# Performance work log

Measured on AMD Instinct MI355X. Metric: run time of the kernel, lower is better.

## Reference

```python
import jax, jax.numpy as jnp
import numpy as np

NUM_PARTS = 16
NUM_K = 256          # num_k_per_part; table rows per part = NUM_K + 1
VAE_DIMS = 768
OUT_DIMS = 1024
B = 4096


def setup_inputs() -> dict:
    key = jax.random.key(0)
    k0, k1, k2, k3, k4 = jax.random.split(key, 5)
    hashes = jax.random.randint(k0, (B, NUM_PARTS), 0, NUM_K + 1)  # values 0..256
    # nn.init.normal_(embedding.weight, 0.0, 0.01)
    emb = jax.random.normal(k1, ((NUM_K + 1) * NUM_PARTS, VAE_DIMS), dtype=jnp.float32) * 0.01
    # projection: Linear(768 -> 1024), ReLU, Linear(1024 -> 1024)
    W1 = jax.random.normal(k2, (VAE_DIMS, OUT_DIMS), dtype=jnp.float32) * (1.0 / np.sqrt(VAE_DIMS))
    b1 = jnp.zeros((OUT_DIMS,), dtype=jnp.float32)
    W2 = jax.random.normal(k3, (OUT_DIMS, OUT_DIMS), dtype=jnp.float32) * (1.0 / np.sqrt(OUT_DIMS))
    b2 = jnp.zeros((OUT_DIMS,), dtype=jnp.float32)
    # pe = randn(num_parts, out_dims) * 1.0
    pe = jax.random.normal(k4, (NUM_PARTS, OUT_DIMS), dtype=jnp.float32)
    return {"hashes": hashes, "emb": emb, "W1": W1, "b1": b1, "W2": W2, "b2": b2, "pe": pe}


def reference(hashes, emb, W1, b1, W2, b2, pe):
    # forward(hashes, index=None, get_mu=False, input_is_mu=False)
    offset = jnp.arange(NUM_PARTS, dtype=hashes.dtype) * (NUM_K + 1)  # [P]
    idx = hashes + offset[None, :]                                    # [B, P]
    mu = emb[idx]                                                     # [B, P, VAE]
    h = jax.nn.relu(jnp.einsum('bpv,vh->bph', mu, W1) + b1)           # [B, P, OUT]
    projected = jnp.einsum('bph,ho->bpo', h, W2) + b2                 # [B, P, OUT]
    return projected + pe[None, :, :]                                 # pe broadcast over batch
```

## Files before the change

kernel.cpp:

```cpp
#include <hip/hip_runtime.h>
#include <stdint.h>

#define NPARTS 16
#define NK1    257
#define ROWS   4112
#define MPAD   4224
#define VAE    768
#define ODIM   1024
#define BROWS  65536

typedef __attribute__((ext_vector_type(4))) float f32x4;
typedef __attribute__((ext_vector_type(8))) short s16x8;

static __device__ __forceinline__ unsigned short f2bf(float f) {
  union { float f; unsigned u; } v; v.f = f;
  unsigned x = v.u;
  unsigned r = x + 0x7FFFu + ((x >> 16) & 1u);
  return (unsigned short)(r >> 16);
}

static __device__ __forceinline__ void gload_lds16(const void* g, void* l) {
  __builtin_amdgcn_global_load_lds(
      (const __attribute__((address_space(1))) unsigned int*)g,
      (__attribute__((address_space(3))) unsigned int*)l, 16, 0, 0);
}

#define EMB_BLOCKS 1024
__global__ __launch_bounds__(256) void prep_kernel(
    const float* __restrict__ emb, const float* __restrict__ W1,
    unsigned short* __restrict__ embB, unsigned short* __restrict__ w1t) {
  __shared__ unsigned short tile[32][33];
  const int tid = threadIdx.x;
  const int bid = blockIdx.x;
  if (bid < EMB_BLOCKS) {
    const int NQ = MPAD * VAE / 4;
    for (int g = bid * 256 + tid; g < NQ; g += EMB_BLOCKS * 256) {
      const int i4 = g * 4;
      ushort4 o;
      if (i4 < ROWS * VAE) {
        const float4 v = *(const float4*)(emb + i4);
        o.x = f2bf(v.x); o.y = f2bf(v.y); o.z = f2bf(v.z); o.w = f2bf(v.w);
      } else {
        o.x = 0; o.y = 0; o.z = 0; o.w = 0;
      }
      *(ushort4*)(embB + i4) = o;
    }
  } else {
    const int tb = bid - EMB_BLOCKS;
    const int nkt = VAE / 32;
    const int tk = (tb % nkt) * 32;
    const int tn = (tb / nkt) * 32;
    const int r  = tid >> 3;
    const int c4 = (tid & 7) * 4;
    const float4 v = *(const float4*)(W1 + (size_t)(tk + r) * ODIM + tn + c4);
    tile[r][c4 + 0] = f2bf(v.x);
    tile[r][c4 + 1] = f2bf(v.y);
    tile[r][c4 + 2] = f2bf(v.z);
    tile[r][c4 + 3] = f2bf(v.w);
    __syncthreads();
    ushort4 o;
    o.x = tile[c4 + 0][r];
    o.y = tile[c4 + 1][r];
    o.z = tile[c4 + 2][r];
    o.w = tile[c4 + 3][r];
    *(ushort4*)(w1t + (size_t)(tn + r) * VAE + tk + c4) = o;
  }
}

template <int K, int MODE, bool DO_W2T>
__global__ __launch_bounds__(256) void gemm_kernel(
    const unsigned short* __restrict__ A, const unsigned short* __restrict__ BT,
    const float* __restrict__ bias, const float* __restrict__ pe,
    unsigned short* __restrict__ outB, float* __restrict__ outF,
    const float* __restrict__ W2src, unsigned short* __restrict__ w2dst) {
  __shared__ __align__(16) unsigned short smem[3 * 12288];
  const int tid = threadIdx.x;

  if (DO_W2T && blockIdx.z == 1) {
    if (blockIdx.y >= 32) return;
    unsigned short (*ttile)[132] = (unsigned short (*)[132])smem;
    const int tk = blockIdx.y * 32, tn = blockIdx.x * 128;
#pragma unroll
    for (int q = 0; q < 4; ++q) {
      const int row = (tid >> 5) + q * 8, c4 = (tid & 31) * 4;
      const float4 v = *(const float4*)(W2src + (size_t)(tk + row) * ODIM + tn + c4);
      ttile[row][c4 + 0] = f2bf(v.x); ttile[row][c4 + 1] = f2bf(v.y);
      ttile[row][c4 + 2] = f2bf(v.z); ttile[row][c4 + 3] = f2bf(v.w);
    }
    __syncthreads();
#pragma unroll
    for (int q = 0; q < 4; ++q) {
      const int n = (tid >> 3) + q * 32, k4 = (tid & 7) * 4;
      ushort4 o;
      o.x = ttile[k4 + 0][n]; o.y = ttile[k4 + 1][n];
      o.z = ttile[k4 + 2][n]; o.w = ttile[k4 + 3][n];
      *(ushort4*)(w2dst + (size_t)(tn + n) * ODIM + tk + k4) = o;
    }
    return;
  }

  const int lane = tid & 63;
  const int wave = tid >> 6;
  const int wc   = wave * 32;
  const int brow = blockIdx.y * 64;
  const int bcol = blockIdx.x * 128;
  const int la   = lane & 15;
  const int hi   = lane >> 4;

  f32x4 acc[4][2];
#pragma unroll
  for (int m = 0; m < 4; ++m)
#pragma unroll
    for (int n = 0; n < 2; ++n)
#pragma unroll
      for (int r = 0; r < 4; ++r) acc[m][n][r] = 0.f;

  const int srow = tid >> 3;
  const int skb  = (tid & 7) ^ (srow & 7);
  const unsigned short* gA = A + (size_t)(brow + srow) * K + skb * 8;
  const unsigned short* gB = BT + (size_t)(bcol + srow) * K + skb * 8;

#define STAGE(b, kt)                                              \
  {                                                               \
    unsigned short* la_ = smem + (b) * 12288 + tid * 8;           \
    unsigned short* lb_ = la_ + 4096;                             \
    gload_lds16(gA + (kt), la_);                                  \
    gload_lds16(gA + (kt) + 32 * K, la_ + 2048);                  \
    gload_lds16(gB + (kt), lb_);                                  \
    gload_lds16(gB + (kt) + 32 * K, lb_ + 2048);                  \
    gload_lds16(gB + (kt) + 64 * K, lb_ + 4096);                  \
    gload_lds16(gB + (kt) + 96 * K, lb_ + 6144);                  \
  }

  const int NT = K / 64;
  STAGE(0, 0);
  STAGE(1, 64);

#pragma unroll
  for (int t = 0; t < NT; ++t) {
    if (t < NT - 1) asm volatile("s_waitcnt vmcnt(6)" ::: "memory");
    else            asm volatile("s_waitcnt vmcnt(0)" ::: "memory");
    __builtin_amdgcn_sched_barrier(0);
    __builtin_amdgcn_s_barrier();
    if (t + 2 < NT) STAGE((t + 2) % 3, (t + 2) * 64);

    const unsigned short* As = smem + (t % 3) * 12288;
    const unsigned short* Bs = As + 4096;
    s16x8 af[4][2], bf[2][2];
#pragma unroll
    for (int m = 0; m < 4; ++m)
#pragma unroll
      for (int ks = 0; ks < 2; ++ks)
        af[m][ks] = *(const s16x8*)(As + (m * 16 + la) * 64 +
                                    (((ks * 4 + hi) ^ (la & 7)) * 8));
#pragma unroll
    for (int n = 0; n < 2; ++n)
#pragma unroll
      for (int ks = 0; ks < 2; ++ks)
        bf[n][ks] = *(const s16x8*)(Bs + (wc + n * 16 + la) * 64 +
                                    (((ks * 4 + hi) ^ (la & 7)) * 8));
    asm volatile("s_waitcnt lgkmcnt(0)" ::: "memory");
    __builtin_amdgcn_sched_barrier(0);

    __builtin_amdgcn_s_setprio(1);
#pragma unroll
    for (int m = 0; m < 4; ++m)
#pragma unroll
      for (int n = 0; n < 2; ++n)
#pragma unroll
        for (int ks = 0; ks < 2; ++ks)
          acc[m][n] = __builtin_amdgcn_mfma_f32_16x16x32_bf16(af[m][ks], bf[n][ks],
                                                              acc[m][n], 0, 0, 0);
    __builtin_amdgcn_s_setprio(0);
  }
#undef STAGE

#pragma unroll
  for (int m = 0; m < 4; ++m) {
    const int row0 = brow + m * 16 + hi * 4;
#pragma unroll
    for (int n = 0; n < 2; ++n) {
      const int col = bcol + wc + n * 16 + la;
      const float bv = bias[col];
      if (MODE == 0) {
#pragma unroll
        for (int r = 0; r < 4; ++r) {
          float v = acc[m][n][r] + bv;
          v = v > 0.f ? v : 0.f;
          outB[(size_t)(row0 + r) * ODIM + col] = f2bf(v);
        }
      } else {
#pragma unroll
        for (int r = 0; r < 4; ++r) {
          const int row = row0 + r;
          int p = row / NK1;
          if (p > NPARTS - 1) p = NPARTS - 1;
          outF[(size_t)row * ODIM + col] = acc[m][n][r] + bv + pe[(size_t)p * ODIM + col];
        }
      }
    }
  }
}

__global__ __launch_bounds__(256) void gather_kernel(const int* __restrict__ hashes,
                                                     const float* __restrict__ T,
                                                     float* __restrict__ out) {
  const int wid  = (blockIdx.x * blockDim.x + threadIdx.x) >> 6;
  const int lane = threadIdx.x & 63;
  const int nw   = (gridDim.x * blockDim.x) >> 6;
  for (int row = wid; row < BROWS; row += nw) {
    const int h = __builtin_amdgcn_readfirstlane(hashes[row]);
    const int p = row & (NPARTS - 1);
    const f32x4* __restrict__ src = (const f32x4*)(T + (size_t)(h + p * NK1) * ODIM);
    f32x4* __restrict__ dst = (f32x4*)(out + (size_t)row * ODIM);
#pragma unroll
    for (int j = 0; j < 4; ++j) {
      f32x4 v = src[lane + j * 64];
      __builtin_nontemporal_store(v, dst + lane + j * 64);
    }
  }
}

extern "C" void kernel_launch(void* const* d_in, const int* in_sizes, int n_in,
                              void* d_out, int out_size, void* d_ws, size_t ws_size,
                              hipStream_t stream) {
  const int*   hashes = (const int*)d_in[0];
  const float* emb    = (const float*)d_in[1];
  const float* W1     = (const float*)d_in[2];
  const float* b1     = (const float*)d_in[3];
  const float* W2     = (const float*)d_in[4];
  const float* b2     = (const float*)d_in[5];
  const float* pe     = (const float*)d_in[6];
  float* out = (float*)d_out;

  char* ws = (char*)d_ws;
  unsigned short* embB = (unsigned short*)(ws);
  unsigned short* w1t  = (unsigned short*)(ws + 6488064);
  unsigned short* w2t  = (unsigned short*)(ws + 8060928);
  unsigned short* H    = (unsigned short*)(ws + 10158080);
  float*          T    = (float*)(ws + 18808832);

  prep_kernel<<<EMB_BLOCKS + 768, 256, 0, stream>>>(emb, W1, embB, w1t);

  gemm_kernel<VAE, 0, true><<<dim3(8, 66, 2), 256, 0, stream>>>(
      embB, w1t, b1, nullptr, H, nullptr, W2, w2t);

  gemm_kernel<ODIM, 2, false><<<dim3(8, 66, 1), 256, 0, stream>>>(
      H, w2t, b2, pe, nullptr, T, nullptr, nullptr);

  gather_kernel<<<2048, 256, 0, stream>>>(hashes, T, out);
}
```

Before: 95.36 us.

## Fuse emb bf16 conversion into GEMM1, simplify pipelines, XCD-localize gather

The separate conversion of the embedding table to bf16 is removed; GEMM1 now reads fp32 emb rows directly, converts them in registers and writes swizzled bf16 into LDS, which saves one full read/write pass over the table. Both GEMMs go from a 3-stage global_load_lds pipeline with explicit waitcnt, setprio and sched_barrier to a simpler 2-stage double buffer using __syncthreads. The gather kernel is remapped so each group of blocks (blockIdx & 7, likely targeting one XCD) handles two parts, improving L2 locality on the T table. The cost is that the A operand now goes through register loads and conversion in the hot loop, and the pipeline is shallower.

```diff
diff --git a/kernel.cpp b/kernel.cpp
--- a/kernel.cpp
+++ b/kernel.cpp
@@ -25,58 +25,38 @@
       (__attribute__((address_space(3))) unsigned int*)l, 16, 0, 0);
 }
 
-#define EMB_BLOCKS 1024
 __global__ __launch_bounds__(256) void prep_kernel(
-    const float* __restrict__ emb, const float* __restrict__ W1,
-    unsigned short* __restrict__ embB, unsigned short* __restrict__ w1t) {
+    const float* __restrict__ W1, unsigned short* __restrict__ w1t) {
   __shared__ unsigned short tile[32][33];
   const int tid = threadIdx.x;
-  const int bid = blockIdx.x;
-  if (bid < EMB_BLOCKS) {
-    const int NQ = MPAD * VAE / 4;
-    for (int g = bid * 256 + tid; g < NQ; g += EMB_BLOCKS * 256) {
-      const int i4 = g * 4;
-      ushort4 o;
-      if (i4 < ROWS * VAE) {
-        const float4 v = *(const float4*)(emb + i4);
-        o.x = f2bf(v.x); o.y = f2bf(v.y); o.z = f2bf(v.z); o.w = f2bf(v.w);
-      } else {
-        o.x = 0; o.y = 0; o.z = 0; o.w = 0;
-      }
-      *(ushort4*)(embB + i4) = o;
-    }
-  } else {
-    const int tb = bid - EMB_BLOCKS;
-    const int nkt = VAE / 32;
-    const int tk = (tb % nkt) * 32;
-    const int tn = (tb / nkt) * 32;
-    const int r  = tid >> 3;
-    const int c4 = (tid & 7) * 4;
-    const float4 v = *(const float4*)(W1 + (size_t)(tk + r) * ODIM + tn + c4);
-    tile[r][c4 + 0] = f2bf(v.x);
-    tile[r][c4 + 1] = f2bf(v.y);
-    tile[r][c4 + 2] = f2bf(v.z);
-    tile[r][c4 + 3] = f2bf(v.w);
-    __syncthreads();
-    ushort4 o;
-    o.x = tile[c4 + 0][r];
-    o.y = tile[c4 + 1][r];
-    o.z = tile[c4 + 2][r];
-    o.w = tile[c4 + 3][r];
-    *(ushort4*)(w1t + (size_t)(tn + r) * VAE + tk + c4) = o;
-  }
-}
-
-template <int K, int MODE, bool DO_W2T>
-__global__ __launch_bounds__(256) void gemm_kernel(
-    const unsigned short* __restrict__ A, const unsigned short* __restrict__ BT,
-    const float* __restrict__ bias, const float* __restrict__ pe,
-    unsigned short* __restrict__ outB, float* __restrict__ outF,
+  const int tb  = blockIdx.x;
+  const int nkt = VAE / 32;
+  const int tk = (tb % nkt) * 32;
+  const int tn = (tb / nkt) * 32;
+  const int r  = tid >> 3;
+  const int c4 = (tid & 7) * 4;
+  const float4 v = *(const float4*)(W1 + (size_t)(tk + r) * ODIM + tn + c4);
+  tile[r][c4 + 0] = f2bf(v.x);
+  tile[r][c4 + 1] = f2bf(v.y);
+  tile[r][c4 + 2] = f2bf(v.z);
+  tile[r][c4 + 3] = f2bf(v.w);
+  __syncthreads();
+  ushort4 o;
+  o.x = tile[c4 + 0][r];
+  o.y = tile[c4 + 1][r];
+  o.z = tile[c4 + 2][r];
+  o.w = tile[c4 + 3][r];
+  *(ushort4*)(w1t + (size_t)(tn + r) * VAE + tk + c4) = o;
+}
+
+__global__ __launch_bounds__(256) void gemm1_kernel(
+    const float* __restrict__ emb, const unsigned short* __restrict__ BT,
+    const float* __restrict__ bias, unsigned short* __restrict__ outB,
     const float* __restrict__ W2src, unsigned short* __restrict__ w2dst) {
-  __shared__ __align__(16) unsigned short smem[3 * 12288];
+  __shared__ __align__(16) unsigned short smem[2 * 12288];
   const int tid = threadIdx.x;
 
-  if (DO_W2T && blockIdx.z == 1) {
+  if (blockIdx.z == 1) {
     if (blockIdx.y >= 32) return;
     unsigned short (*ttile)[132] = (unsigned short (*)[132])smem;
     const int tk = blockIdx.y * 32, tn = blockIdx.x * 128;
@@ -106,6 +86,115 @@
   const int bcol = blockIdx.x * 128;
   const int la   = lane & 15;
   const int hi   = lane >> 4;
+
+  f32x4 acc[4][2];
+#pragma unroll
+  for (int m = 0; m < 4; ++m)
+#pragma unroll
+    for (int n = 0; n < 2; ++n)
+#pragma unroll
+      for (int r = 0; r < 4; ++r) acc[m][n][r] = 0.f;
+
+  const int srow = tid >> 3;
+  const int skb  = (tid & 7) ^ (srow & 7);
+  const unsigned short* gB = BT + (size_t)(bcol + srow) * VAE + skb * 8;
+  const int arow = tid >> 2;
+  const int ak   = (tid & 3) * 16;
+  const int kb0  = ((tid & 3) * 2) ^ (arow & 7);
+  const int kb1  = ((tid & 3) * 2 + 1) ^ (arow & 7);
+  const bool aok = (brow + arow) < ROWS;
+  const float* gA = emb + (size_t)(brow + arow) * VAE + ak;
+
+  auto stage = [&](int b, int kt) {
+    unsigned short* lb_ = smem + b * 12288 + 4096 + tid * 8;
+    gload_lds16(gB + kt, lb_);
+    gload_lds16(gB + kt + 32 * VAE, lb_ + 2048);
+    gload_lds16(gB + kt + 64 * VAE, lb_ + 4096);
+    gload_lds16(gB + kt + 96 * VAE, lb_ + 6144);
+    float4 f0, f1, f2, f3;
+    if (aok) {
+      f0 = *(const float4*)(gA + kt);
+      f1 = *(const float4*)(gA + kt + 4);
+      f2 = *(const float4*)(gA + kt + 8);
+      f3 = *(const float4*)(gA + kt + 12);
+    } else {
+      f0 = f1 = f2 = f3 = float4{0.f, 0.f, 0.f, 0.f};
+    }
+    s16x8 p0, p1;
+    p0[0] = f2bf(f0.x); p0[1] = f2bf(f0.y); p0[2] = f2bf(f0.z); p0[3] = f2bf(f0.w);
+    p0[4] = f2bf(f1.x); p0[5] = f2bf(f1.y); p0[6] = f2bf(f1.z); p0[7] = f2bf(f1.w);
+    p1[0] = f2bf(f2.x); p1[1] = f2bf(f2.y); p1[2] = f2bf(f2.z); p1[3] = f2bf(f2.w);
+    p1[4] = f2bf(f3.x); p1[5] = f2bf(f3.y); p1[6] = f2bf(f3.z); p1[7] = f2bf(f3.w);
+    unsigned short* la_ = smem + b * 12288 + arow * 64;
+    *(s16x8*)(la_ + kb0 * 8) = p0;
+    *(s16x8*)(la_ + kb1 * 8) = p1;
+  };
+
+  stage(0, 0);
+  __syncthreads();
+
+  const int NT = VAE / 64;
+  for (int t = 0; t < NT; ++t) {
+    const int cur = t & 1;
+    if (t + 1 < NT) stage(cur ^ 1, (t + 1) * 64);
+
+    const unsigned short* As = smem + cur * 12288;
+    const unsigned short* Bs = As + 4096;
+    s16x8 af[4][2], bf[2][2];
+#pragma unroll
+    for (int m = 0; m < 4; ++m)
+#pragma unroll
+      for (int ks = 0; ks < 2; ++ks)
+        af[m][ks] = *(const s16x8*)(As + (m * 16 + la) * 64 +
+                                    (((ks * 4 + hi) ^ (la & 7)) * 8));
+#pragma unroll
+    for (int n = 0; n < 2; ++n)
+#pragma unroll
+      for (int ks = 0; ks < 2; ++ks)
+        bf[n][ks] = *(const s16x8*)(Bs + (wc + n * 16 + la) * 64 +
+                                    (((ks * 4 + hi) ^ (la & 7)) * 8));
+#pragma unroll
+    for (int m = 0; m < 4; ++m)
+#pragma unroll
+      for (int n = 0; n < 2; ++n)
+#pragma unroll
+        for (int ks = 0; ks < 2; ++ks)
+          acc[m][n] = __builtin_amdgcn_mfma_f32_16x16x32_bf16(af[m][ks], bf[n][ks],
+                                                              acc[m][n], 0, 0, 0);
+    __syncthreads();
+  }
+
+#pragma unroll
+  for (int m = 0; m < 4; ++m) {
+    const int row0 = brow + m * 16 + hi * 4;
+#pragma unroll
+    for (int n = 0; n < 2; ++n) {
+      const int col = bcol + wc + n * 16 + la;
+      const float bv = bias[col];
+#pragma unroll
+      for (int r = 0; r < 4; ++r) {
+        float v = acc[m][n][r] + bv;
+        v = v > 0.f ? v : 0.f;
+        outB[(size_t)(row0 + r) * ODIM + col] = f2bf(v);
+      }
+    }
+  }
+}
+
+__global__ __launch_bounds__(256) void gemm2_kernel(
+    const unsigned short* __restrict__ A, const unsigned short* __restrict__ BT,
+    const float* __restrict__ bias, const float* __restrict__ pe,
+    float* __restrict__ outF) {
+  __shared__ __align__(16) unsigned short smem[2 * 12288];
+  const int tid  = threadIdx.x;
+  const int lane = tid & 63;
+  const int wave = tid >> 6;
+  const int wc   = wave * 32;
+  const int brow = blockIdx.y * 64;
+  const int bcol = blockIdx.x * 128;
+  const int la   = lane & 15;
+  const int hi   = lane >> 4;
+  const int K    = ODIM;
 
   f32x4 acc[4][2];
 #pragma unroll
@@ -132,19 +221,15 @@
     gload_lds16(gB + (kt) + 96 * K, lb_ + 6144);                  \
   }
 
+  STAGE(0, 0);
+  __syncthreads();
+
   const int NT = K / 64;
-  STAGE(0, 0);
-  STAGE(1, 64);
-
-#pragma unroll
   for (int t = 0; t < NT; ++t) {
-    if (t < NT - 1) asm volatile("s_waitcnt vmcnt(6)" ::: "memory");
-    else            asm volatile("s_waitcnt vmcnt(0)" ::: "memory");
-    __builtin_amdgcn_sched_barrier(0);
-    __builtin_amdgcn_s_barrier();
-    if (t + 2 < NT) STAGE((t + 2) % 3, (t + 2) * 64);
-
-    const unsigned short* As = smem + (t % 3) * 12288;
+    const int cur = t & 1;
+    if (t + 1 < NT) STAGE(cur ^ 1, (t + 1) * 64);
+
+    const unsigned short* As = smem + cur * 12288;
     const unsigned short* Bs = As + 4096;
     s16x8 af[4][2], bf[2][2];
 #pragma unroll
@@ -159,10 +244,6 @@
       for (int ks = 0; ks < 2; ++ks)
         bf[n][ks] = *(const s16x8*)(Bs + (wc + n * 16 + la) * 64 +
                                     (((ks * 4 + hi) ^ (la & 7)) * 8));
-    asm volatile("s_waitcnt lgkmcnt(0)" ::: "memory");
-    __builtin_amdgcn_sched_barrier(0);
-
-    __builtin_amdgcn_s_setprio(1);
 #pragma unroll
     for (int m = 0; m < 4; ++m)
 #pragma unroll
@@ -171,7 +252,7 @@
         for (int ks = 0; ks < 2; ++ks)
           acc[m][n] = __builtin_amdgcn_mfma_f32_16x16x32_bf16(af[m][ks], bf[n][ks],
                                                               acc[m][n], 0, 0, 0);
-    __builtin_amdgcn_s_setprio(0);
+    __syncthreads();
   }
 #undef STAGE
 
@@ -182,21 +263,12 @@
     for (int n = 0; n < 2; ++n) {
       const int col = bcol + wc + n * 16 + la;
       const float bv = bias[col];
-      if (MODE == 0) {
-#pragma unroll
-        for (int r = 0; r < 4; ++r) {
-          float v = acc[m][n][r] + bv;
-          v = v > 0.f ? v : 0.f;
-          outB[(size_t)(row0 + r) * ODIM + col] = f2bf(v);
-        }
-      } else {
-#pragma unroll
-        for (int r = 0; r < 4; ++r) {
-          const int row = row0 + r;
-          int p = row / NK1;
-          if (p > NPARTS - 1) p = NPARTS - 1;
-          outF[(size_t)row * ODIM + col] = acc[m][n][r] + bv + pe[(size_t)p * ODIM + col];
-        }
+#pragma unroll
+      for (int r = 0; r < 4; ++r) {
+        const int row = row0 + r;
+        int p = row / NK1;
+        if (p > NPARTS - 1) p = NPARTS - 1;
+        outF[(size_t)row * ODIM + col] = acc[m][n][r] + bv + pe[(size_t)p * ODIM + col];
       }
     }
   }
@@ -205,14 +277,21 @@
 __global__ __launch_bounds__(256) void gather_kernel(const int* __restrict__ hashes,
                                                      const float* __restrict__ T,
                                                      float* __restrict__ out) {
-  const int wid  = (blockIdx.x * blockDim.x + threadIdx.x) >> 6;
+  const int xcd  = blockIdx.x & 7;
+  const int bi   = blockIdx.x >> 3;
+  const int wave = threadIdx.x >> 6;
   const int lane = threadIdx.x & 63;
-  const int nw   = (gridDim.x * blockDim.x) >> 6;
-  for (int row = wid; row < BROWS; row += nw) {
-    const int h = __builtin_amdgcn_readfirstlane(hashes[row]);
-    const int p = row & (NPARTS - 1);
+  const int wl   = bi * 4 + wave;
+  const int p0   = xcd * 2;
+#pragma unroll
+  for (int i = 0; i < 8; ++i) {
+    const int r     = wl + i * 1024;
+    const int batch = r >> 1;
+    const int p     = p0 + (r & 1);
+    const int orow  = batch * NPARTS + p;
+    const int h = __builtin_amdgcn_readfirstlane(hashes[orow]);
     const f32x4* __restrict__ src = (const f32x4*)(T + (size_t)(h + p * NK1) * ODIM);
-    f32x4* __restrict__ dst = (f32x4*)(out + (size_t)row * ODIM);
+    f32x4* __restrict__ dst = (f32x4*)(out + (size_t)orow * ODIM);
 #pragma unroll
     for (int j = 0; j < 4; ++j) {
       f32x4 v = src[lane + j * 64];
@@ -234,19 +313,16 @@
   float* out = (float*)d_out;
 
   char* ws = (char*)d_ws;
-  unsigned short* embB = (unsigned short*)(ws);
-  unsigned short* w1t  = (unsigned short*)(ws + 6488064);
-  unsigned short* w2t  = (unsigned short*)(ws + 8060928);
-  unsigned short* H    = (unsigned short*)(ws + 10158080);
-  float*          T    = (float*)(ws + 18808832);
-
-  prep_kernel<<<EMB_BLOCKS + 768, 256, 0, stream>>>(emb, W1, embB, w1t);
-
-  gemm_kernel<VAE, 0, true><<<dim3(8, 66, 2), 256, 0, stream>>>(
-      embB, w1t, b1, nullptr, H, nullptr, W2, w2t);
-
-  gemm_kernel<ODIM, 2, false><<<dim3(8, 66, 1), 256, 0, stream>>>(
-      H, w2t, b2, pe, nullptr, T, nullptr, nullptr);
+  unsigned short* w1t = (unsigned short*)(ws);
+  unsigned short* w2t = (unsigned short*)(ws + 1572864);
+  unsigned short* H   = (unsigned short*)(ws + 3670016);
+  float*          T   = (float*)(ws + 12320768);
+
+  prep_kernel<<<768, 256, 0, stream>>>(W1, w1t);
+
+  gemm1_kernel<<<dim3(8, 66, 2), 256, 0, stream>>>(emb, w1t, b1, H, W2, w2t);
+
+  gemm2_kernel<<<dim3(8, 66, 1), 256, 0, stream>>>(H, w2t, b2, pe, T);
 
   gather_kernel<<<2048, 256, 0, stream>>>(hashes, T, out);
 }
```

Result: no change. 97.06 us (+1.8%).
